# Optimization experiments

Hardware: AMD Instinct MI355X
Metric: run time of the kernel (lower is better)

The kernel has to match this reference:

```python
import jax, jax.numpy as jnp
import numpy as np

JITTER = 0.01  # router_noise


def setup_inputs() -> dict:
    key = jax.random.key(0)
    ks = jax.random.split(key, 8)
    B, H, W, D = 4, 32, 64, 512
    E, F = 8, 2048
    N = B * H * W
    s = lambda fan: 1.0 / np.sqrt(fan)
    return {
        "input_data": jax.random.normal(ks[0], (B, H, W, D), dtype=jnp.float32),
        "attr": jax.random.normal(ks[1], (N, 3), dtype=jnp.float32),
        "Wr": jax.random.normal(ks[2], (3, E), dtype=jnp.float32) * s(3),
        "br": jnp.zeros((E,), dtype=jnp.float32),
        "W1": jax.random.normal(ks[3], (E, D, F), dtype=jnp.float32) * s(D),
        "b1": jnp.zeros((E, F), dtype=jnp.float32),
        "W2": jax.random.normal(ks[4], (E, F, D), dtype=jnp.float32) * s(F),
        "b2": jnp.zeros((E, D), dtype=jnp.float32),
    }


def reference(input_data, attr, Wr, br, W1, b1, W2, b2):
    B, H, W_, D = input_data.shape
    E = W1.shape[0]
    x = input_data.reshape(-1, D)  # [N, D]

    # --- Top1Router with multiplicative jitter noise in [1-eps, 1+eps] ---
    u = jax.random.uniform(jax.random.key(42), attr.shape, dtype=attr.dtype)
    noisy_attr = attr * ((1.0 + JITTER) - 2.0 * JITTER * u)
    router_logits = noisy_attr @ Wr + br                   # [N, E]
    router_probs = jax.nn.softmax(router_logits, axis=-1)  # [N, E]
    routes = jnp.argmax(router_probs, axis=-1)             # [N] int
    route_prob_max = jnp.max(router_probs, axis=-1)        # [N]

    # --- Dispatch to top-1 expert (eval: no capacity dropping) ---
    # Fixed small loop over experts; masked dense compute (jit-friendly,
    # no data-dependent shapes).
    out = jnp.zeros_like(x)
    for i in range(E):
        h = jax.nn.gelu(x @ W1[i] + b1[i], approximate=False)  # [N, F]
        y = h @ W2[i] + b2[i]                                  # [N, D]
        out = jnp.where((routes == i)[:, None], y, out)

    # is_scale_prob=True: scale output by the max routing probability
    out = out * route_prob_max[:, None]
    return out.reshape(B, H, W_, D)
```

## Files before the change

### kernel.cpp

```cpp
#include <hip/hip_runtime.h>
#include <hip/hip_bf16.h>

typedef unsigned int u32;
typedef __bf16 bf16x8 __attribute__((ext_vector_type(8)));
typedef float  f32x4  __attribute__((ext_vector_type(4)));

#define NTOK 8192
#define DIM  512
#define FDIM 2048
#define NEXP 8

#define OFF_W1T   0ull
#define OFF_W2T   16777216ull
#define OFF_XB    33554432ull
#define OFF_H     41943040ull
#define OFF_SCALE 75497472ull
#define OFF_CNT   75530240ull
#define OFF_LIST  75530272ull

__device__ __forceinline__ u32 rotl32(u32 x, int r) { return (x << r) | (x >> (32 - r)); }

__device__ __forceinline__ void threefry2x32(u32 k0, u32 k1, u32 x0, u32 x1,
                                             u32& y0, u32& y1) {
  u32 ks2 = k0 ^ k1 ^ 0x1BD11BDAu;
  x0 += k0; x1 += k1;
#define TF_RND(r) { x0 += x1; x1 = rotl32(x1, r); x1 ^= x0; }
  TF_RND(13) TF_RND(15) TF_RND(26) TF_RND(6)
  x0 += k1;  x1 += ks2 + 1u;
  TF_RND(17) TF_RND(29) TF_RND(16) TF_RND(24)
  x0 += ks2; x1 += k0 + 2u;
  TF_RND(13) TF_RND(15) TF_RND(26) TF_RND(6)
  x0 += k0;  x1 += k1 + 3u;
  TF_RND(17) TF_RND(29) TF_RND(16) TF_RND(24)
  x0 += k1;  x1 += ks2 + 4u;
  TF_RND(13) TF_RND(15) TF_RND(26) TF_RND(6)
  x0 += ks2; x1 += k0 + 5u;
#undef TF_RND
  y0 = x0; y1 = x1;
}

__device__ __forceinline__ float jax_uniform(u32 j) {
  u32 y0, y1;
  threefry2x32(0u, 42u, 0u, j, y0, y1);
  u32 bits = y0 ^ y1;
  return __uint_as_float((bits >> 9) | 0x3F800000u) - 1.0f;
}

__device__ __forceinline__ unsigned short f2b(float f) {
  u32 u = __float_as_uint(f);
  u32 r = (u + 0x7FFFu + ((u >> 16) & 1u)) >> 16;
  return (unsigned short)r;
}

__global__ __launch_bounds__(256) void router_kernel(
    const float* __restrict__ attr, const float* __restrict__ Wr,
    const float* __restrict__ br, float* __restrict__ scale,
    int* __restrict__ cnt, int* __restrict__ list) {
  int i = blockIdx.x * 256 + threadIdx.x;
  if (i >= NTOK) return;
  float a[3];
#pragma unroll
  for (int c = 0; c < 3; ++c) {
    float u = jax_uniform((u32)(3 * i + c));
    a[c] = attr[3 * i + c] * ((1.0f + 0.01f) - 2.0f * 0.01f * u);
  }
  float logits[NEXP];
#pragma unroll
  for (int e = 0; e < NEXP; ++e)
    logits[e] = br[e] + a[0] * Wr[0 * NEXP + e] + a[1] * Wr[1 * NEXP + e] + a[2] * Wr[2 * NEXP + e];
  float m = logits[0]; int am = 0;
#pragma unroll
  for (int e = 1; e < NEXP; ++e)
    if (logits[e] > m) { m = logits[e]; am = e; }
  float s = 0.f;
#pragma unroll
  for (int e = 0; e < NEXP; ++e) s += expf(logits[e] - m);
  scale[i] = 1.0f / s;
  int pos = atomicAdd(&cnt[am], 1);
  list[am * NTOK + pos] = i;
}

__global__ __launch_bounds__(256) void convert_x_kernel(const float4* __restrict__ in,
                                                        uint2* __restrict__ out) {
  int i = blockIdx.x * 256 + threadIdx.x;
  if (i >= NTOK * DIM / 4) return;
  float4 v = in[i];
  u32 lo = (u32)f2b(v.x) | ((u32)f2b(v.y) << 16);
  u32 hi = (u32)f2b(v.z) | ((u32)f2b(v.w) << 16);
  out[i] = make_uint2(lo, hi);
}

__global__ __launch_bounds__(256) void transpose_bf16_kernel(
    const float* __restrict__ in, unsigned short* __restrict__ out, int R, int C) {
  int e = blockIdx.z;
  in  += (size_t)e * R * C;
  out += (size_t)e * R * C;
  __shared__ float tile[32][33];
  int c0 = blockIdx.x * 32, r0 = blockIdx.y * 32;
  int tr = threadIdx.x >> 5;
  int tc = threadIdx.x & 31;
#pragma unroll
  for (int it = 0; it < 4; ++it)
    tile[tr + it * 8][tc] = in[(size_t)(r0 + tr + it * 8) * C + c0 + tc];
  __syncthreads();
#pragma unroll
  for (int it = 0; it < 4; ++it)
    out[(size_t)(c0 + tr + it * 8) * R + r0 + tc] = f2b(tile[tc][tr + it * 8]);
}

__device__ __forceinline__ void load_lds16(const void* g, void* l) {
  __builtin_amdgcn_global_load_lds(
      (const __attribute__((address_space(1))) u32*)g,
      (__attribute__((address_space(3))) u32*)l, 16, 0, 0);
}

template <int KK, int NN, bool G1, int SPLITK>
__global__ __launch_bounds__(256, 4) void moe_gemm_kernel(
    const unsigned short* __restrict__ A,
    const unsigned short* __restrict__ Bt,
    const float* __restrict__ bias,
    const int* __restrict__ list,
    const int* __restrict__ cnt,
    const float* __restrict__ scale,
    unsigned short* __restrict__ Hout,
    float* __restrict__ Yout) {
  const int e = blockIdx.z % NEXP;
  const int chunk = blockIdx.z / NEXP;
  const int cn = cnt[e];
  const int m0 = blockIdx.y * 128;
  if (m0 >= cn) return;
  const int n0 = blockIdx.x * 128;
  const int tid = threadIdx.x;
  const int lane = tid & 63;
  const int wid = tid >> 6;
  const int wm = wid >> 1, wn = wid & 1;

  constexpr int KC = KK / SPLITK;
  constexpr int NSTEP = KC / 32;
  const int k_base = chunk * KC;

  __shared__ __align__(16) unsigned short SM[2 * 8192];

  const int* mylist = list + e * NTOK;
  const unsigned short* Be = Bt + (size_t)e * NN * KK;

  int aoff[2], boff[2], ldso[2];
#pragma unroll
  for (int j = 0; j < 2; ++j) {
    int o = j * 4096 + tid * 16;
    int row = o >> 6;
    int slot = (o >> 4) & 3;
    int g = (slot - (row >> 1)) & 3;
    int p = m0 + row; if (p >= cn) p = cn - 1;
    int tok = mylist[p];
    aoff[j] = tok * KK + g * 8 + k_base;
    boff[j] = (n0 + row) * KK + g * 8 + k_base;
    ldso[j] = o;
  }

  f32x4 acc[4][4];
#pragma unroll
  for (int i = 0; i < 4; ++i)
#pragma unroll
    for (int j = 0; j < 4; ++j) acc[i][j] = (f32x4){0.f, 0.f, 0.f, 0.f};

  int a_addr[4], b_addr[4];
#pragma unroll
  for (int mi = 0; mi < 4; ++mi) {
    int row = wm * 64 + mi * 16 + (lane & 15);
    int gp = ((lane >> 4) + (row >> 1)) & 3;
    a_addr[mi] = (row * 32 + gp * 8) * 2;
  }
#pragma unroll
  for (int ni = 0; ni < 4; ++ni) {
    int row = wn * 64 + ni * 16 + (lane & 15);
    int gp = ((lane >> 4) + (row >> 1)) & 3;
    b_addr[ni] = (row * 32 + gp * 8) * 2;
  }

#define STAGE(kt, b)                                                        \
  {                                                                         \
    int koff = (kt) * 32;                                                   \
    char* base = (char*)SM + (b) * 16384;                                   \
    _Pragma("unroll")                                                       \
    for (int j = 0; j < 2; ++j) {                                           \
      load_lds16(A + aoff[j] + koff, base + ldso[j]);                       \
      load_lds16(Be + boff[j] + koff, base + 8192 + ldso[j]);               \
    }                                                                       \
  }

#define COMPUTE(b)                                                          \
  {                                                                         \
    const char* base = (const char*)SM + (b) * 16384;                       \
    bf16x8 af[4], bfr[4];                                                   \
    _Pragma("unroll")                                                       \
    for (int mi = 0; mi < 4; ++mi) af[mi] = *(const bf16x8*)(base + a_addr[mi]); \
    _Pragma("unroll")                                                       \
    for (int ni = 0; ni < 4; ++ni) bfr[ni] = *(const bf16x8*)(base + 8192 + b_addr[ni]); \
    _Pragma("unroll")                                                       \
    for (int mi = 0; mi < 4; ++mi)                                          \
      _Pragma("unroll")                                                     \
      for (int ni = 0; ni < 4; ++ni)                                        \
        acc[mi][ni] = __builtin_amdgcn_mfma_f32_16x16x32_bf16(af[mi], bfr[ni], acc[mi][ni], 0, 0, 0); \
  }

  STAGE(0, 0)
  __syncthreads();
  int cur = 0;
  for (int kt = 0; kt < NSTEP - 1; ++kt) {
    STAGE(kt + 1, cur ^ 1)
    COMPUTE(cur)
    __syncthreads();
    cur ^= 1;
  }
  COMPUTE(cur)
#undef STAGE
#undef COMPUTE

  const int colb = n0 + wn * 64 + (lane & 15);
  float bia[4];
#pragma unroll
  for (int ni = 0; ni < 4; ++ni) bia[ni] = bias[(size_t)e * NN + colb + ni * 16];
#pragma unroll
  for (int mi = 0; mi < 4; ++mi) {
#pragma unroll
    for (int i = 0; i < 4; ++i) {
      int p = m0 + wm * 64 + mi * 16 + (lane >> 4) * 4 + i;
      if (p < cn) {
        int tok = mylist[p];
        if constexpr (G1) {
#pragma unroll
          for (int ni = 0; ni < 4; ++ni) {
            float v = acc[mi][ni][i] + bia[ni];
            float g = 0.5f * v * (1.0f + erff(v * 0.70710678118654752f));
            Hout[(size_t)tok * NN + colb + ni * 16] = f2b(g);
          }
        } else {
          float s = scale[tok];
#pragma unroll
          for (int ni = 0; ni < 4; ++ni) {
            float v = acc[mi][ni][i] + (chunk == 0 ? bia[ni] : 0.0f);
            unsafeAtomicAdd(&Yout[(size_t)tok * NN + colb + ni * 16], v * s);
          }
        }
      }
    }
  }
}

extern "C" void kernel_launch(void* const* d_in, const int* in_sizes, int n_in,
                              void* d_out, int out_size, void* d_ws, size_t ws_size,
                              hipStream_t stream) {
  const float* x    = (const float*)d_in[0];
  const float* attr = (const float*)d_in[1];
  const float* Wr   = (const float*)d_in[2];
  const float* br   = (const float*)d_in[3];
  const float* W1   = (const float*)d_in[4];
  const float* b1   = (const float*)d_in[5];
  const float* W2   = (const float*)d_in[6];
  const float* b2   = (const float*)d_in[7];
  float* out = (float*)d_out;
  char* ws = (char*)d_ws;

  unsigned short* W1t = (unsigned short*)(ws + OFF_W1T);
  unsigned short* W2t = (unsigned short*)(ws + OFF_W2T);
  unsigned short* xb  = (unsigned short*)(ws + OFF_XB);
  unsigned short* H   = (unsigned short*)(ws + OFF_H);
  float* scale        = (float*)(ws + OFF_SCALE);
  int* cnt            = (int*)(ws + OFF_CNT);
  int* list           = (int*)(ws + OFF_LIST);

  hipMemsetAsync(cnt, 0, NEXP * sizeof(int), stream);
  hipMemsetAsync(out, 0, (size_t)out_size * sizeof(float), stream);
  router_kernel<<<NTOK / 256, 256, 0, stream>>>(attr, Wr, br, scale, cnt, list);
  convert_x_kernel<<<(NTOK * DIM / 4) / 256, 256, 0, stream>>>((const float4*)x, (uint2*)xb);
  transpose_bf16_kernel<<<dim3(FDIM / 32, DIM / 32, NEXP), 256, 0, stream>>>(W1, W1t, DIM, FDIM);
  transpose_bf16_kernel<<<dim3(DIM / 32, FDIM / 32, NEXP), 256, 0, stream>>>(W2, W2t, FDIM, DIM);

  moe_gemm_kernel<DIM, FDIM, true, 1><<<dim3(FDIM / 128, NTOK / 128, NEXP), 256, 0, stream>>>(
      xb, W1t, b1, list, cnt, scale, H, nullptr);
  moe_gemm_kernel<FDIM, DIM, false, 4><<<dim3(DIM / 128, NTOK / 128, NEXP * 4), 256, 0, stream>>>(
      H, W2t, b2, list, cnt, scale, nullptr, out);
}
```

Before: 209.5 us.

## Pre-gather routed tokens into contiguous padded blocks and compact the GEMM grid

Measured after the change: 245.5 us. 17.2% more time.

```diff
diff --git a/kernel.cpp b/kernel.cpp
--- a/kernel.cpp
+++ b/kernel.cpp
@@ -9,14 +9,17 @@
 #define DIM  512
 #define FDIM 2048
 #define NEXP 8
-
-#define OFF_W1T   0ull
-#define OFF_W2T   16777216ull
-#define OFF_XB    33554432ull
-#define OFF_H     41943040ull
-#define OFF_SCALE 75497472ull
-#define OFF_CNT   75530240ull
-#define OFF_LIST  75530272ull
+#define NRB_MAX 72
+#define NPAD (NRB_MAX * 128)
+
+#define OFF_WT    0ull
+#define OFF_XG    16777216ull
+#define OFF_H     26214400ull
+#define OFF_SCALE 63963136ull
+#define OFF_CNT   63995904ull
+#define OFF_RBEXP 63996032ull
+#define OFF_LIST  63996416ull
+#define OFF_GLIST 64258560ull
 
 __device__ __forceinline__ u32 rotl32(u32 x, int r) { return (x << r) | (x >> (32 - r)); }
 
@@ -80,14 +83,57 @@
   list[am * NTOK + pos] = i;
 }
 
-__global__ __launch_bounds__(256) void convert_x_kernel(const float4* __restrict__ in,
-                                                        uint2* __restrict__ out) {
-  int i = blockIdx.x * 256 + threadIdx.x;
-  if (i >= NTOK * DIM / 4) return;
-  float4 v = in[i];
-  u32 lo = (u32)f2b(v.x) | ((u32)f2b(v.y) << 16);
-  u32 hi = (u32)f2b(v.z) | ((u32)f2b(v.w) << 16);
-  out[i] = make_uint2(lo, hi);
+__global__ __launch_bounds__(256) void setup_kernel(
+    const int* __restrict__ cnt, const int* __restrict__ list,
+    int* __restrict__ rbexp, int* __restrict__ glist) {
+  __shared__ int sp[NEXP], srb[NEXP], sc[NEXP];
+  if (threadIdx.x == 0) {
+    int off = 0, rb = 0;
+    for (int e = 0; e < NEXP; ++e) {
+      sp[e] = off; srb[e] = rb; sc[e] = cnt[e];
+      int nb = (sc[e] + 127) >> 7;
+      off += nb << 7; rb += nb;
+    }
+  }
+  __syncthreads();
+  for (int rb = threadIdx.x; rb < NRB_MAX; rb += 256) {
+    int e2 = -1;
+    for (int q = 0; q < NEXP; ++q) {
+      int nb = (sc[q] + 127) >> 7;
+      if (rb >= srb[q] && rb < srb[q] + nb) e2 = q;
+    }
+    rbexp[rb] = e2;
+  }
+  for (int p = threadIdx.x; p < NPAD; p += 256) {
+    int v = -1;
+    for (int q = 0; q < NEXP; ++q) {
+      int nb = (sc[q] + 127) >> 7;
+      int i = p - sp[q];
+      if (i >= 0 && i < (nb << 7)) v = (i < sc[q]) ? list[q * NTOK + i] : -1;
+    }
+    glist[p] = v;
+  }
+}
+
+__global__ __launch_bounds__(256) void gather_kernel(
+    const float* __restrict__ x, const int* __restrict__ glist,
+    uint4* __restrict__ xg) {
+  int idx = blockIdx.x * 256 + threadIdx.x;
+  if (idx >= NPAD * (DIM / 8)) return;
+  int p = idx >> 6;
+  int c = (idx & 63) * 8;
+  int tok = glist[p];
+  uint4 o = {0u, 0u, 0u, 0u};
+  if (tok >= 0) {
+    const float* s = x + (size_t)tok * DIM + c;
+    float4 v0 = *(const float4*)s;
+    float4 v1 = *(const float4*)(s + 4);
+    o.x = (u32)f2b(v0.x) | ((u32)f2b(v0.y) << 16);
+    o.y = (u32)f2b(v0.z) | ((u32)f2b(v0.w) << 16);
+    o.z = (u32)f2b(v1.x) | ((u32)f2b(v1.y) << 16);
+    o.w = (u32)f2b(v1.z) | ((u32)f2b(v1.w) << 16);
+  }
+  xg[idx] = o;
 }
 
 __global__ __launch_bounds__(256) void transpose_bf16_kernel(
@@ -115,20 +161,19 @@
 }
 
 template <int KK, int NN, bool G1, int SPLITK>
-__global__ __launch_bounds__(256, 4) void moe_gemm_kernel(
+__global__ __launch_bounds__(256, 5) void moe_gemm_kernel(
     const unsigned short* __restrict__ A,
     const unsigned short* __restrict__ Bt,
     const float* __restrict__ bias,
-    const int* __restrict__ list,
-    const int* __restrict__ cnt,
+    const int* __restrict__ rbexp,
+    const int* __restrict__ glist,
     const float* __restrict__ scale,
     unsigned short* __restrict__ Hout,
     float* __restrict__ Yout) {
-  const int e = blockIdx.z % NEXP;
-  const int chunk = blockIdx.z / NEXP;
-  const int cn = cnt[e];
-  const int m0 = blockIdx.y * 128;
-  if (m0 >= cn) return;
+  const int e = rbexp[blockIdx.y];
+  if (e < 0) return;
+  const int chunk = blockIdx.z;
+  const int r0 = blockIdx.y * 128;
   const int n0 = blockIdx.x * 128;
   const int tid = threadIdx.x;
   const int lane = tid & 63;
@@ -139,9 +184,8 @@
   constexpr int NSTEP = KC / 32;
   const int k_base = chunk * KC;
 
-  __shared__ __align__(16) unsigned short SM[2 * 8192];
-
-  const int* mylist = list + e * NTOK;
+  __shared__ __align__(16) char SM[2 * 16384];
+
   const unsigned short* Be = Bt + (size_t)e * NN * KK;
 
   int aoff[2], boff[2], ldso[2];
@@ -151,9 +195,7 @@
     int row = o >> 6;
     int slot = (o >> 4) & 3;
     int g = (slot - (row >> 1)) & 3;
-    int p = m0 + row; if (p >= cn) p = cn - 1;
-    int tok = mylist[p];
-    aoff[j] = tok * KK + g * 8 + k_base;
+    aoff[j] = (r0 + row) * KK + g * 8 + k_base;
     boff[j] = (n0 + row) * KK + g * 8 + k_base;
     ldso[j] = o;
   }
@@ -225,17 +267,17 @@
   for (int mi = 0; mi < 4; ++mi) {
 #pragma unroll
     for (int i = 0; i < 4; ++i) {
-      int p = m0 + wm * 64 + mi * 16 + (lane >> 4) * 4 + i;
-      if (p < cn) {
-        int tok = mylist[p];
-        if constexpr (G1) {
-#pragma unroll
-          for (int ni = 0; ni < 4; ++ni) {
-            float v = acc[mi][ni][i] + bia[ni];
-            float g = 0.5f * v * (1.0f + erff(v * 0.70710678118654752f));
-            Hout[(size_t)tok * NN + colb + ni * 16] = f2b(g);
-          }
-        } else {
+      int p = r0 + wm * 64 + mi * 16 + (lane >> 4) * 4 + i;
+      if constexpr (G1) {
+#pragma unroll
+        for (int ni = 0; ni < 4; ++ni) {
+          float v = acc[mi][ni][i] + bia[ni];
+          float g = 0.5f * v * (1.0f + erff(v * 0.70710678118654752f));
+          Hout[(size_t)p * NN + colb + ni * 16] = f2b(g);
+        }
+      } else {
+        int tok = glist[p];
+        if (tok >= 0) {
           float s = scale[tok];
 #pragma unroll
           for (int ni = 0; ni < 4; ++ni) {
@@ -262,23 +304,25 @@
   float* out = (float*)d_out;
   char* ws = (char*)d_ws;
 
-  unsigned short* W1t = (unsigned short*)(ws + OFF_W1T);
-  unsigned short* W2t = (unsigned short*)(ws + OFF_W2T);
-  unsigned short* xb  = (unsigned short*)(ws + OFF_XB);
+  unsigned short* WT  = (unsigned short*)(ws + OFF_WT);
+  unsigned short* xg  = (unsigned short*)(ws + OFF_XG);
   unsigned short* H   = (unsigned short*)(ws + OFF_H);
   float* scale        = (float*)(ws + OFF_SCALE);
   int* cnt            = (int*)(ws + OFF_CNT);
+  int* rbexp          = (int*)(ws + OFF_RBEXP);
   int* list           = (int*)(ws + OFF_LIST);
+  int* glist          = (int*)(ws + OFF_GLIST);
 
   hipMemsetAsync(cnt, 0, NEXP * sizeof(int), stream);
   hipMemsetAsync(out, 0, (size_t)out_size * sizeof(float), stream);
   router_kernel<<<NTOK / 256, 256, 0, stream>>>(attr, Wr, br, scale, cnt, list);
-  convert_x_kernel<<<(NTOK * DIM / 4) / 256, 256, 0, stream>>>((const float4*)x, (uint2*)xb);
-  transpose_bf16_kernel<<<dim3(FDIM / 32, DIM / 32, NEXP), 256, 0, stream>>>(W1, W1t, DIM, FDIM);
-  transpose_bf16_kernel<<<dim3(DIM / 32, FDIM / 32, NEXP), 256, 0, stream>>>(W2, W2t, FDIM, DIM);
-
-  moe_gemm_kernel<DIM, FDIM, true, 1><<<dim3(FDIM / 128, NTOK / 128, NEXP), 256, 0, stream>>>(
-      xb, W1t, b1, list, cnt, scale, H, nullptr);
-  moe_gemm_kernel<FDIM, DIM, false, 4><<<dim3(DIM / 128, NTOK / 128, NEXP * 4), 256, 0, stream>>>(
-      H, W2t, b2, list, cnt, scale, nullptr, out);
-}
+  setup_kernel<<<1, 256, 0, stream>>>(cnt, list, rbexp, glist);
+  gather_kernel<<<(NPAD * (DIM / 8)) / 256, 256, 0, stream>>>(x, glist, (uint4*)xg);
+
+  transpose_bf16_kernel<<<dim3(FDIM / 32, DIM / 32, NEXP), 256, 0, stream>>>(W1, WT, DIM, FDIM);
+  moe_gemm_kernel<DIM, FDIM, true, 1><<<dim3(FDIM / 128, NRB_MAX, 1), 256, 0, stream>>>(
+      xg, WT, b1, rbexp, glist, scale, H, nullptr);
+  transpose_bf16_kernel<<<dim3(DIM / 32, FDIM / 32, NEXP), 256, 0, stream>>>(W2, WT, FDIM, DIM);
+  moe_gemm_kernel<FDIM, DIM, false, 4><<<dim3(DIM / 128, NRB_MAX, 4), 256, 0, stream>>>(
+      H, WT, b2, rbexp, glist, scale, nullptr, out);
+}
```
